# Kernel optimization log

Hardware: AMD Instinct MI355X
Metric: run time of the kernel (lower is better)

The kernel has to match this reference:

```python
import jax, jax.numpy as jnp
import numpy as np
import math

E = 256      # embed_dim
H = 16       # num_heads
D = E // H   # qkv_dim
MSH = 16     # ms_hidden_dim
B, R, C = 2, 512, 512


def setup_inputs() -> dict:
    key = jax.random.key(0)
    ks = jax.random.split(key, 10)
    x1 = jax.random.normal(ks[0], (B, R, E), jnp.float32)
    x2 = jax.random.normal(ks[1], (B, C, E), jnp.float32)
    attn_mask = jax.random.randint(ks[2], (B, R, C), 0, 2) > 0  # True = valid
    cost_mat = jax.random.uniform(ks[3], (B, R, C), jnp.float32)
    # torch nn.Linear default init ~ U(-1/sqrt(fan_in), 1/sqrt(fan_in))
    def lin(k, out_d, in_d, bound):
        return jax.random.uniform(k, (out_d, in_d), jnp.float32, -bound, bound)
    Wqv1 = lin(ks[4], 2 * E, E, 1.0 / math.sqrt(E))
    Wkv2 = lin(ks[5], 2 * E, E, 1.0 / math.sqrt(E))
    W1 = lin(ks[6], H * MSH, 2 * H, math.sqrt(0.5))       # mix1_init
    W2 = lin(ks[7], H, H * MSH, math.sqrt(1.0 / MSH))      # mix2_init
    Wout1 = lin(ks[8], E, E, 1.0 / math.sqrt(E))
    Wout2 = lin(ks[9], E, E, 1.0 / math.sqrt(E))
    return {"x1": x1, "x2": x2, "attn_mask": attn_mask, "cost_mat": cost_mat,
            "Wqv1": Wqv1, "Wkv2": Wkv2, "W1": W1, "W2": W2,
            "Wout1": Wout1, "Wout2": Wout2}


def _apply_weights_and_combine(logits, v, mask):
    # mask: True = masked out; rows fully masked are un-masked (torch clone trick)
    all_masked = jnp.all(mask, axis=-1, keepdims=True)
    mask = jnp.where(all_masked, False, mask)
    logits = jnp.where(mask, -jnp.inf, logits)
    w = jax.nn.softmax(logits, axis=-1)          # [b,h,r,c]
    out = jnp.einsum('bhrc,bhcd->bhrd', w, v)     # [b,h,r,d]
    b, h, r, d = out.shape
    return out.transpose(0, 2, 1, 3).reshape(b, r, h * d)  # b s (h d)


def reference(x1, x2, attn_mask, cost_mat, Wqv1, Wkv2, W1, W2, Wout1, Wout2):
    b, r, _ = x1.shape
    c = x2.shape[1]
    # q, v1 from x1 ; k, v2 from x2
    qv = (x1 @ Wqv1.T).reshape(b, r, 2, H, D)
    q = qv[:, :, 0].transpose(0, 2, 1, 3)   # [b,h,r,d]
    v1 = qv[:, :, 1].transpose(0, 2, 1, 3)
    kv = (x2 @ Wkv2.T).reshape(b, c, 2, H, D)
    k = kv[:, :, 0].transpose(0, 2, 1, 3)   # [b,h,c,d]
    v2 = kv[:, :, 1].transpose(0, 2, 1, 3)

    dot = jnp.einsum('bhrd,bhcd->bhrc', q, k) * (1.0 / math.sqrt(D))
    cost = jnp.broadcast_to(cost_mat[:, None], dot.shape)  # [b,h,r,c]

    # MixedScoreFF: stack -> [b,h,r,c,2] -> [b,r,c,2h] -> MLP -> [b,r,c,h]
    two = jnp.stack((dot, cost), axis=-1)
    two = two.transpose(0, 2, 3, 1, 4).reshape(b, r, c, 2 * H)
    ms = jax.nn.relu(two @ W1.T) @ W2.T      # [b,r,c,H]
    ms1 = ms.transpose(0, 3, 1, 2)            # [b,h,r,c]
    ms2 = ms1.transpose(0, 1, 3, 2)           # [b,h,c,r]

    mask1 = jnp.broadcast_to(~attn_mask[:, None], (b, H, r, c))  # True = masked
    mask2 = mask1.transpose(0, 1, 3, 2)

    h1 = _apply_weights_and_combine(ms1, v2, mask1) @ Wout1.T  # [b,r,E]
    h2 = _apply_weights_and_combine(ms2, v1, mask2) @ Wout2.T  # [b,c,E]
    return (h1, h2)
```

## Files before the change

kernel.cpp:

```cpp
#include <hip/hip_runtime.h>
#include <hip/hip_bf16.h>

typedef unsigned int   u32;
typedef unsigned short u16;

typedef __attribute__((ext_vector_type(8))) short    sh8;
typedef __attribute__((ext_vector_type(4))) float    f32x4;
typedef __attribute__((ext_vector_type(8))) _Float16 f16x8;
typedef __attribute__((ext_vector_type(2))) _Float16 f16x2;
typedef __attribute__((ext_vector_type(2))) __fp16   fp16x2raw;

union F16x8 { f16x8 v; uint4 u; f16x2 p[4]; _Float16 h[8]; };
union F16x4u { uint2 u; _Float16 h[4]; };
union F16x2u { u32 u; _Float16 h[2]; };
union CvtU  { fp16x2raw r; f16x2 p; u32 u; };

__device__ __forceinline__ float b2f(u16 u) { union { u32 i; float f; } v; v.i = ((u32)u) << 16; return v.f; }
__device__ __forceinline__ u16   f2b(float f){
  union { float f; u32 i; } v; v.f = f;
  u32 u = v.i;
  u32 r = (u + 0x7fffu + ((u >> 16) & 1u)) >> 16;
  return (u16)r;
}
__device__ __forceinline__ u32 pk2(float a, float b) {
  __hip_bfloat162 h2 = __float22bfloat162_rn(make_float2(a, b));
  union { __hip_bfloat162 h; u32 u; } v; v.h = h2; return v.u;
}
__device__ __forceinline__ f16x2 cvtpk(float a, float b) {
  CvtU c; c.r = __builtin_amdgcn_cvt_pkrtz(a, b); return c.p;
}
__device__ __forceinline__ u32 cvtpku(float a, float b) {
  CvtU c; c.r = __builtin_amdgcn_cvt_pkrtz(a, b); return c.u;
}

__device__ __forceinline__ f32x4 mfma16(uint4 a, uint4 b, f32x4 c) {
  union { uint4 u; sh8 s; } ua, ub;
  ua.u = a; ub.u = b;
  return __builtin_amdgcn_mfma_f32_16x16x32_bf16(ua.s, ub.s, c, 0, 0, 0);
}
__device__ __forceinline__ f32x4 mfma32h(f16x8 a, f16x8 b, f32x4 c) {
  return __builtin_amdgcn_mfma_f32_16x16x32_f16(a, b, c, 0, 0, 0);
}

__device__ __forceinline__ void split8(float4 v0, float4 v1, uint4& hi, uint4& lo) {
  float a[8] = {v0.x, v0.y, v0.z, v0.w, v1.x, v1.y, v1.z, v1.w};
  u32 hw[4], lw[4];
#pragma unroll
  for (int t = 0; t < 4; t++) {
    u32 hp = pk2(a[2 * t], a[2 * t + 1]);
    float r0 = a[2 * t]     - __uint_as_float(hp << 16);
    float r1 = a[2 * t + 1] - __uint_as_float(hp & 0xffff0000u);
    hw[t] = hp;
    lw[t] = pk2(r0, r1);
  }
  hi = make_uint4(hw[0], hw[1], hw[2], hw[3]);
  lo = make_uint4(lw[0], lw[1], lw[2], lw[3]);
}

__global__ void __launch_bounds__(256)
gemm_mf(const float* __restrict__ A0, const float* __restrict__ B0, float* __restrict__ C0,
        const float* __restrict__ A1, const float* __restrict__ B1, float* __restrict__ C1,
        int N, int K) {
  int t = threadIdx.x, L = t & 63, w = t >> 6;
  int cl = L & 15, q = L >> 4;
  int by = blockIdx.y, sel = by >> 4;
  const float* A  = sel ? A1 : A0;
  const float* Bw = sel ? B1 : B0;
  float*       C  = sel ? C1 : C0;
  int m0 = (by & 15) * 64 + w * 16;
  int n0 = blockIdx.x * 16;

  f32x4 acc; acc[0] = 0.f; acc[1] = 0.f; acc[2] = 0.f; acc[3] = 0.f;
  const float* ar = A  + (size_t)(m0 + cl) * K + 8 * q;
  const float* br = Bw + (size_t)(n0 + cl) * K + 8 * q;

  for (int k0 = 0; k0 < K; k0 += 32) {
    float4 av0 = *(const float4*)(ar + k0);
    float4 av1 = *(const float4*)(ar + k0 + 4);
    float4 bv0 = *(const float4*)(br + k0);
    float4 bv1 = *(const float4*)(br + k0 + 4);
    uint4 ahi, alo, bhi, blo;
    split8(av0, av1, ahi, alo);
    split8(bv0, bv1, bhi, blo);
    acc = mfma16(ahi, bhi, acc);
    acc = mfma16(ahi, blo, acc);
    acc = mfma16(alo, bhi, acc);
  }
#pragma unroll
  for (int i = 0; i < 4; i++)
    C[(size_t)(m0 + 4 * q + i) * N + n0 + cl] = acc[i];
}

__global__ void __launch_bounds__(256)
gemm_mf_pack(const float* __restrict__ x1, const float* __restrict__ Wqv1, u16* __restrict__ vhT1,
             const float* __restrict__ x2, const float* __restrict__ Wkv2, u16* __restrict__ vhT2,
             const float* __restrict__ W1, const float* __restrict__ W2,
             uint4* __restrict__ QQ4, uint4* __restrict__ KH4, uint4* __restrict__ KL4z,
             uint4* __restrict__ W1F8hi, uint4* __restrict__ W1F8lo,
             uint4* __restrict__ W2F8hi, uint4* __restrict__ W2F8lo) {
  __shared__ float Ld[4][16][17];
  int t = threadIdx.x, L = t & 63, w = t >> 6;
  int cl = L & 15, q = L >> 4;
  int by = blockIdx.y;

  if (by == 32) {
    if (blockIdx.x >= 8) return;
    int tid = blockIdx.x * 256 + t;
    if (tid < 1024) {
      int LL = tid & 63, nt = tid >> 6;
      int j = nt * 16 + (LL & 15), qq = LL >> 4;
      F16x8 hi, lo;
#pragma unroll
      for (int jj = 0; jj < 8; jj++) {
        float wv = W1[j * 32 + qq * 8 + jj];
        hi.h[jj] = (_Float16)wv;
        lo.h[jj] = (_Float16)(wv - (float)hi.h[jj]);
      }
      W1F8hi[tid] = hi.u;
      W1F8lo[tid] = lo.u;
    } else if (tid < 1536) {
      int t2 = tid - 1024;
      int LL = t2 & 63, p = t2 >> 6;
      int h = LL & 15, qq = LL >> 4;
      F16x8 hi, lo;
#pragma unroll
      for (int jj = 0; jj < 8; jj++) {
        int j = 32 * p + ((jj >> 2) << 4) + 4 * qq + (jj & 3);
        float wv = W2[h * 256 + j];
        hi.h[jj] = (_Float16)wv;
        lo.h[jj] = (_Float16)(wv - (float)hi.h[jj]);
      }
      W2F8hi[t2] = hi.u;
      W2F8lo[t2] = lo.u;
    }
    return;
  }

  int sel = by >> 4;
  const float* A  = sel ? x2 : x1;
  const float* Bw = sel ? Wkv2 : Wqv1;
  int m0 = (by & 15) * 64 + w * 16;
  int n0 = blockIdx.x * 16;

  f32x4 acc; acc[0] = 0.f; acc[1] = 0.f; acc[2] = 0.f; acc[3] = 0.f;
  const float* ar = A  + (size_t)(m0 + cl) * 256 + 8 * q;
  const float* br = Bw + (size_t)(n0 + cl) * 256 + 8 * q;

  for (int k0 = 0; k0 < 256; k0 += 32) {
    float4 av0 = *(const float4*)(ar + k0);
    float4 av1 = *(const float4*)(ar + k0 + 4);
    float4 bv0 = *(const float4*)(br + k0);
    float4 bv1 = *(const float4*)(br + k0 + 4);
    uint4 ahi, alo, bhi, blo;
    split8(av0, av1, ahi, alo);
    split8(bv0, bv1, bhi, blo);
    acc = mfma16(ahi, bhi, acc);
    acc = mfma16(ahi, blo, acc);
    acc = mfma16(alo, bhi, acc);
  }

  int b = m0 >> 9;
  int row = (m0 & 511) + cl;

  if (n0 >= 256) {
#pragma unroll
    for (int i = 0; i < 4; i++) Ld[w][cl][4 * q + i] = acc[i];
    if (q < 2) {
      float vt[8];
#pragma unroll
      for (int jj = 0; jj < 8; jj++) vt[jj] = Ld[w][cl][q * 8 + jj];
      uint4 o = make_uint4(cvtpku(vt[0], vt[1]), cvtpku(vt[2], vt[3]),
                           cvtpku(vt[4], vt[5]), cvtpku(vt[6], vt[7]));
      u16* vT = sel ? vhT2 : vhT1;
      *(uint4*)(vT + ((size_t)(b * 256) + (n0 - 256) + cl) * 512 + (m0 & 511) + 8 * q) = o;
    }
    return;
  }

#pragma unroll
  for (int i = 0; i < 4; i++) Ld[w][cl][4 * q + i] = acc[i];
  float v[8];
#pragma unroll
  for (int jj = 0; jj < 8; jj++) v[jj] = Ld[w][(q & 1) * 8 + jj][cl];

  int r = row;
  int h = n0 >> 4;

  if (sel == 0) {
    u32 wv[4];
#pragma unroll
    for (int t2 = 0; t2 < 4; t2++) {
      float a  = v[2 * t2] * 0.25f, bb = v[2 * t2 + 1] * 0.25f;
      u32 hp = pk2(a, bb);
      if (q >= 2) {
        float r0 = a  - __uint_as_float(hp << 16);
        float r1 = bb - __uint_as_float(hp & 0xffff0000u);
        wv[t2] = pk2(r0, r1);
      } else wv[t2] = hp;
    }
    QQ4[((size_t)((b * 16 + h) * 4 + q) << 9) + r] = make_uint4(wv[0], wv[1], wv[2], wv[3]);
  } else {
    u32 hw[4], lw[4];
#pragma unroll
    for (int t2 = 0; t2 < 4; t2++) {
      float a = v[2 * t2], bb = v[2 * t2 + 1];
      u32 hp = pk2(a, bb);
      float r0 = a  - __uint_as_float(hp << 16);
      float r1 = bb - __uint_as_float(hp & 0xffff0000u);
      hw[t2] = hp;
      lw[t2] = pk2(r0, r1);
    }
    if (q < 2) {
      KH4[((size_t)((b * 16 + h) * 2 + q) << 9) + r]       = make_uint4(hw[0], hw[1], hw[2], hw[3]);
      KL4z[((size_t)((b * 16 + h) * 4 + 2 + q) << 9) + r]  = make_uint4(0, 0, 0, 0);
    } else {
      KL4z[((size_t)((b * 16 + h) * 4 + (q - 2)) << 9) + r] = make_uint4(lw[0], lw[1], lw[2], lw[3]);
    }
  }
}

__global__ void __launch_bounds__(256, 4)
ms_mfma8c(const uint4* __restrict__ QQ4, const uint4* __restrict__ KH4,
          const uint4* __restrict__ KL4z, const float* __restrict__ cost,
          const uint4* __restrict__ W1F8hi, const uint4* __restrict__ W1F8lo,
          const uint4* __restrict__ W2F8hi, const uint4* __restrict__ W2F8lo,
          u16* __restrict__ ms1, u16* __restrict__ ms2) {
  __shared__ __align__(16) u32 Dl[2 * 2176];
  int t = threadIdx.x, L = t & 63, w = t >> 6;
  int cl = L & 15, q = L >> 4;
  int b = blockIdx.z, c0 = blockIdx.y * 16;
  int pairId = w >> 1, wl = w & 1;
  int r0a = blockIdx.x * 32 + pairId * 16;
  int r0  = r0a + wl * 8;
  u32* D = Dl + pairId * 2176;

  f32x4 z; z[0] = 0.f; z[1] = 0.f; z[2] = 0.f; z[3] = 0.f;

#pragma unroll 2
  for (int hpi = 0; hpi < 4; hpi++) {
    int hp = wl * 4 + hpi;
    int h0 = 2 * hp, h1 = 2 * hp + 1;
    uint4 qa  = QQ4[((size_t)((b * 16 + h0) * 4 + q) << 9) + r0a + cl];
    uint4 qa2 = QQ4[((size_t)((b * 16 + h0) * 4 + (q & 1)) << 9) + r0a + cl];
    uint4 kb1 = KH4[((size_t)((b * 16 + h0) * 2 + (q & 1)) << 9) + c0 + cl];
    uint4 kb2 = KL4z[((size_t)((b * 16 + h0) * 4 + q) << 9) + c0 + cl];
    f32x4 d0 = mfma16(qa, kb1, z);
    d0 = mfma16(qa2, kb2, d0);
    uint4 qb  = QQ4[((size_t)((b * 16 + h1) * 4 + q) << 9) + r0a + cl];
    uint4 qb2 = QQ4[((size_t)((b * 16 + h1) * 4 + (q & 1)) << 9) + r0a + cl];
    uint4 kc1 = KH4[((size_t)((b * 16 + h1) * 2 + (q & 1)) << 9) + c0 + cl];
    uint4 kc2 = KL4z[((size_t)((b * 16 + h1) * 4 + q) << 9) + c0 + cl];
    f32x4 d1 = mfma16(qb, kc1, z);
    d1 = mfma16(qb2, kc2, d1);
#pragma unroll
    for (int i = 0; i < 4; i++)
      D[(4 * q + i) * 136 + hp * 17 + cl] = cvtpku(d0[i], d1[i]);
  }
  __syncthreads();

  F16x8 xv[8];
#pragma unroll
  for (int rr = 0; rr < 8; rr++) {
    int rl = wl * 8 + rr;
    float cv = cost[((size_t)(b * 512) + r0 + rr) * 512 + c0 + cl];
    u32 ch = cvtpku(0.f, cv);
    u32 ua = D[rl * 136 + (2 * q) * 17 + cl];
    u32 ub = D[rl * 136 + (2 * q + 1) * 17 + cl];
    xv[rr].u = make_uint4((ua & 0xffffu) | ch, (ua >> 16) | ch,
                          (ub & 0xffffu) | ch, (ub >> 16) | ch);
  }

  f32x4 acc2[8];
#pragma unroll
  for (int rr = 0; rr < 8; rr++) acc2[rr] = z;

#pragma unroll 1
  for (int p = 0; p < 8; p++) {
    F16x8 w1h0, w1h1, w2h, w2l;
    w1h0.u = W1F8hi[(2 * p) * 64 + L];
    w1h1.u = W1F8hi[(2 * p + 1) * 64 + L];
    w2h.u  = W2F8hi[p * 64 + L];
    w2l.u  = W2F8lo[p * 64 + L];
#pragma unroll
    for (int rr = 0; rr < 8; rr++) {
      f32x4 a0 = mfma32h(w1h0.v, xv[rr].v, z);
      f32x4 a1 = mfma32h(w1h1.v, xv[rr].v, z);
      F16x8 hf;
      hf.p[0] = cvtpk(fmaxf(a0[0], 0.f), fmaxf(a0[1], 0.f));
      hf.p[1] = cvtpk(fmaxf(a0[2], 0.f), fmaxf(a0[3], 0.f));
      hf.p[2] = cvtpk(fmaxf(a1[0], 0.f), fmaxf(a1[1], 0.f));
      hf.p[3] = cvtpk(fmaxf(a1[2], 0.f), fmaxf(a1[3], 0.f));
      acc2[rr] = mfma32h(hf.v, w2h.v, acc2[rr]);
      acc2[rr] = mfma32h(hf.v, w2l.v, acc2[rr]);
    }
  }

  u32* ms1u = (u32*)ms1;
#pragma unroll
  for (int rr = 0; rr < 8; rr++) {
    size_t base = ((size_t)(b * 16 + cl) * 512 + (r0 + rr)) * 256 + (c0 >> 1) + q * 2;
    ms1u[base]     = pk2(acc2[rr][0], acc2[rr][1]);
    ms1u[base + 1] = pk2(acc2[rr][2], acc2[rr][3]);
  }
  u32* ms2u = (u32*)ms2;
#pragma unroll
  for (int i = 0; i < 4; i++) {
    int c = c0 + 4 * q + i;
    u32 o[4];
#pragma unroll
    for (int j = 0; j < 4; j++)
      o[j] = pk2(acc2[2 * j][i], acc2[2 * j + 1][i]);
    size_t base2 = ((size_t)(b * 16 + cl) * 512 + c) * 256 + (r0 >> 1);
    *(uint4*)&ms2u[base2] = make_uint4(o[0], o[1], o[2], o[3]);
  }
}

__global__ void __launch_bounds__(256, 4)
softmax_pv_mf(const u16* __restrict__ ms1s, const u16* __restrict__ ms2s,
              const int* __restrict__ mask,
              const u16* __restrict__ vhT1, const u16* __restrict__ vhT2,
              float* __restrict__ o1, float* __restrict__ o2) {
  __shared__ __align__(16) char pbufc[4][8192];
  __shared__ unsigned char maskbytes[8][64];
  __shared__ float sden[4][8];
  int t = threadIdx.x, L = t & 63, w = t >> 6;
  int cl = L & 15, q = L >> 4;
  int bx = blockIdx.x;
  int u  = (bx & 7) + 8 * ((bx >> 3) & 1);
  int v  = (bx >> 4) & 3;
  int hq = bx >> 6;
  int rt = u * 4 + v;
  int b = blockIdx.y, dir = blockIdx.z;
  int fix0 = rt * 8, h = hq * 4 + w;
  const u16* ms = dir ? ms2s : ms1s;

  if (dir == 0) {
#pragma unroll
    for (int fo = 0; fo < 2; fo++) {
      int f = 2 * w + fo;
      const int* mr = mask + ((size_t)(b * 512) + fix0 + f) * 512 + 8 * L;
      uint4 m0 = *(const uint4*)mr;
      uint4 m1 = *(const uint4*)(mr + 4);
      u32 bits = (u32)(m0.x != 0)        | ((u32)(m0.y != 0) << 1)
               | ((u32)(m0.z != 0) << 2) | ((u32)(m0.w != 0) << 3)
               | ((u32)(m1.x != 0) << 4) | ((u32)(m1.y != 0) << 5)
               | ((u32)(m1.z != 0) << 6) | ((u32)(m1.w != 0) << 7);
      maskbytes[f][L] = (unsigned char)bits;
    }
  } else {
    u32 b0 = 0, b1 = 0;
#pragma unroll
    for (int j = 0; j < 8; j++) {
      const int* mp = mask + ((size_t)(b * 512) + 8 * L + j) * 512 + fix0 + 2 * w;
      uint2 mv = *(const uint2*)mp;
      b0 |= (u32)(mv.x != 0) << j;
      b1 |= (u32)(mv.y != 0) << j;
    }
    maskbytes[2 * w][L]     = (unsigned char)b0;
    maskbytes[2 * w + 1][L] = (unsigned char)b1;
  }
  __syncthreads();

  const u16* msbase = ms + ((size_t)((b * 16 + h) * 512) + fix0) * 512 + 8 * L;
  uint4 pre[8];
#pragma unroll
  for (int f = 0; f < 8; f++) pre[f] = *(const uint4*)(msbase + f * 512);

  char* pb = pbufc[w];
#pragma unroll
  for (int f = 0; f < 8; f++) {
    u32 uw[4] = {pre[f].x, pre[f].y, pre[f].z, pre[f].w};
    float lg[8];
#pragma unroll
    for (int j = 0; j < 4; j++) {
      lg[2 * j]     = __uint_as_float(uw[j] << 16);
      lg[2 * j + 1] = __uint_as_float(uw[j] & 0xffff0000u);
    }
    u32 mb = (u32)maskbytes[f][L];
    bool um = (__ballot(mb != 0) != 0ULL);
    u32 eff = um ? mb : 0xffu;
    float mx = -3.4e38f;
#pragma unroll
    for (int j = 0; j < 8; j++)
      mx = fmaxf(mx, ((eff >> j) & 1) ? lg[j] : -3.4e38f);
    for (int off = 32; off; off >>= 1) mx = fmaxf(mx, __shfl_xor(mx, off));
    float s = 0.f; u32 pw[4];
#pragma unroll
    for (int j = 0; j < 4; j++) {
      float p0 = ((eff >> (2 * j)) & 1)     ? __expf(lg[2 * j]     - mx) : 0.f;
      float p1 = ((eff >> (2 * j + 1)) & 1) ? __expf(lg[2 * j + 1] - mx) : 0.f;
      s += p0 + p1;
      pw[j] = cvtpku(p0, p1);
    }
    for (int off = 32; off; off >>= 1) s += __shfl_xor(s, off);
    if (L == 0) sden[w][f] = s;
    *(uint4*)(pb + f * 1024 + ((16 * L) ^ (f << 4))) = make_uint4(pw[0], pw[1], pw[2], pw[3]);
  }

  const u16* vT = (dir ? vhT1 : vhT2) + ((size_t)(b * 256 + h * 16 + cl) * 512) + 8 * q;
  f32x4 accA; accA[0] = 0.f; accA[1] = 0.f; accA[2] = 0.f; accA[3] = 0.f;
  f32x4 accB = accA;
  int ar = (cl & 7);
#pragma unroll
  for (int kk = 0; kk < 16; kk++) {
    F16x8 pa, vb;
    pa.u = *(const uint4*)(pb + ar * 1024 + (((kk << 6) + (q << 4)) ^ (ar << 4)));
    vb.u = *(const uint4*)(vT + (kk << 5));
    if (kk & 1) accB = mfma32h(pa.v, vb.v, accB);
    else        accA = mfma32h(pa.v, vb.v, accA);
  }

  if (q < 2) {
    float* obuf = dir ? o2 : o1;
#pragma unroll
    for (int i = 0; i < 4; i++) {
      int f = 4 * q + i;
      float inv = 1.f / sden[w][f];
      obuf[((size_t)(b * 512) + fix0 + f) * 256 + h * 16 + cl] = (accA[i] + accB[i]) * inv;
    }
  }
}

extern "C" void kernel_launch(void* const* d_in, const int* in_sizes, int n_in,
                              void* d_out, int out_size, void* d_ws, size_t ws_size,
                              hipStream_t stream) {
  const float* x1    = (const float*)d_in[0];
  const float* x2    = (const float*)d_in[1];
  const int*   attn  = (const int*)d_in[2];
  const float* cost  = (const float*)d_in[3];
  const float* Wqv1  = (const float*)d_in[4];
  const float* Wkv2  = (const float*)d_in[5];
  const float* W1    = (const float*)d_in[6];
  const float* W2    = (const float*)d_in[7];
  const float* Wout1 = (const float*)d_in[8];
  const float* Wout2 = (const float*)d_in[9];
  float* out = (float*)d_out;

  char* ws = (char*)d_ws;
  uint4* W1F8hi = (uint4*)(ws);
  uint4* W1F8lo = (uint4*)(ws + (16 << 10));
  uint4* W2F8hi = (uint4*)(ws + (32 << 10));
  uint4* W2F8lo = (uint4*)(ws + (40 << 10));
  u16*   vhT1 = (u16*)(ws + (64 << 10));
  u16*   vhT2 = (u16*)(ws + (64 << 10) + (512 << 10));
  u16*   ms1 = (u16*)(ws + (64 << 10) + (4 << 20));
  u16*   ms2 = (u16*)(ws + (64 << 10) + (20 << 20));
  char*  tail= (ws + (64 << 10) + (36 << 20));
  uint4* QQ4  = (uint4*)(tail);
  uint4* KH4  = (uint4*)(tail + (1 << 20));
  uint4* KL4z = (uint4*)(tail + (1 << 20) + (512 << 10));
  float* o1  = (float*)(tail + (3 << 20));
  float* o2  = (float*)(tail + (4 << 20));

  gemm_mf_pack<<<dim3(32, 33), 256, 0, stream>>>(x1, Wqv1, vhT1, x2, Wkv2, vhT2,
                                                 W1, W2, QQ4, KH4, KL4z,
                                                 W1F8hi, W1F8lo, W2F8hi, W2F8lo);

  ms_mfma8c<<<dim3(16, 32, 2), 256, 0, stream>>>(QQ4, KH4, KL4z, cost,
                                                 W1F8hi, W1F8lo, W2F8hi, W2F8lo, ms1, ms2);

  softmax_pv_mf<<<dim3(256, 2, 2), 256, 0, stream>>>(ms1, ms2, attn, vhT1, vhT2, o1, o2);

  gemm_mf<<<dim3(16, 32), 256, 0, stream>>>(o1, Wout1, out, o2, Wout2, out + (size_t)262144, 256, 256);
}
```

Before: 141.9 us.

## Fuse softmax-PV with output projection into single kernel

Merges the softmax/PV kernel and the output projection GEMM into one kernel. Each 512-thread block now handles all 16 heads for 8 rows, looping over two heads per wave. It stores the normalized attention output as bf16 hi/lo pairs in shared memory and then does the Wout projection from there. This removes one launch and the fp32 o1/o2 round trip through global memory. In exchange the grid drops from 1024 to 256 blocks, and each block re-reads the full Wout matrix, which may hurt occupancy and parallelism.

```diff
diff --git a/kernel.cpp b/kernel.cpp
--- a/kernel.cpp
+++ b/kernel.cpp
@@ -55,40 +55,6 @@
   }
   hi = make_uint4(hw[0], hw[1], hw[2], hw[3]);
   lo = make_uint4(lw[0], lw[1], lw[2], lw[3]);
-}
-
-__global__ void __launch_bounds__(256)
-gemm_mf(const float* __restrict__ A0, const float* __restrict__ B0, float* __restrict__ C0,
-        const float* __restrict__ A1, const float* __restrict__ B1, float* __restrict__ C1,
-        int N, int K) {
-  int t = threadIdx.x, L = t & 63, w = t >> 6;
-  int cl = L & 15, q = L >> 4;
-  int by = blockIdx.y, sel = by >> 4;
-  const float* A  = sel ? A1 : A0;
-  const float* Bw = sel ? B1 : B0;
-  float*       C  = sel ? C1 : C0;
-  int m0 = (by & 15) * 64 + w * 16;
-  int n0 = blockIdx.x * 16;
-
-  f32x4 acc; acc[0] = 0.f; acc[1] = 0.f; acc[2] = 0.f; acc[3] = 0.f;
-  const float* ar = A  + (size_t)(m0 + cl) * K + 8 * q;
-  const float* br = Bw + (size_t)(n0 + cl) * K + 8 * q;
-
-  for (int k0 = 0; k0 < K; k0 += 32) {
-    float4 av0 = *(const float4*)(ar + k0);
-    float4 av1 = *(const float4*)(ar + k0 + 4);
-    float4 bv0 = *(const float4*)(br + k0);
-    float4 bv1 = *(const float4*)(br + k0 + 4);
-    uint4 ahi, alo, bhi, blo;
-    split8(av0, av1, ahi, alo);
-    split8(bv0, bv1, bhi, blo);
-    acc = mfma16(ahi, bhi, acc);
-    acc = mfma16(ahi, blo, acc);
-    acc = mfma16(alo, bhi, acc);
-  }
-#pragma unroll
-  for (int i = 0; i < 4; i++)
-    C[(size_t)(m0 + 4 * q + i) * N + n0 + cl] = acc[i];
 }
 
 __global__ void __launch_bounds__(256)
@@ -315,108 +281,136 @@
   }
 }
 
-__global__ void __launch_bounds__(256, 4)
-softmax_pv_mf(const u16* __restrict__ ms1s, const u16* __restrict__ ms2s,
-              const int* __restrict__ mask,
-              const u16* __restrict__ vhT1, const u16* __restrict__ vhT2,
-              float* __restrict__ o1, float* __restrict__ o2) {
-  __shared__ __align__(16) char pbufc[4][8192];
+__global__ void __launch_bounds__(512, 4)
+softmax_pv_out(const u16* __restrict__ ms1s, const u16* __restrict__ ms2s,
+               const int* __restrict__ mask,
+               const u16* __restrict__ vhT1, const u16* __restrict__ vhT2,
+               const float* __restrict__ Wout1, const float* __restrict__ Wout2,
+               float* __restrict__ out) {
+  __shared__ __align__(16) char pbufc[8][8192];
   __shared__ unsigned char maskbytes[8][64];
-  __shared__ float sden[4][8];
+  __shared__ float sden[8][8];
+  __shared__ __align__(16) u16 ohi[8][264];
+  __shared__ __align__(16) u16 olo[8][264];
   int t = threadIdx.x, L = t & 63, w = t >> 6;
   int cl = L & 15, q = L >> 4;
   int bx = blockIdx.x;
   int u  = (bx & 7) + 8 * ((bx >> 3) & 1);
-  int v  = (bx >> 4) & 3;
-  int hq = bx >> 6;
-  int rt = u * 4 + v;
+  int v  = bx >> 4;
   int b = blockIdx.y, dir = blockIdx.z;
-  int fix0 = rt * 8, h = hq * 4 + w;
+  int fix0 = (u * 4 + v) * 8;
   const u16* ms = dir ? ms2s : ms1s;
 
   if (dir == 0) {
-#pragma unroll
-    for (int fo = 0; fo < 2; fo++) {
-      int f = 2 * w + fo;
-      const int* mr = mask + ((size_t)(b * 512) + fix0 + f) * 512 + 8 * L;
-      uint4 m0 = *(const uint4*)mr;
-      uint4 m1 = *(const uint4*)(mr + 4);
-      u32 bits = (u32)(m0.x != 0)        | ((u32)(m0.y != 0) << 1)
-               | ((u32)(m0.z != 0) << 2) | ((u32)(m0.w != 0) << 3)
-               | ((u32)(m1.x != 0) << 4) | ((u32)(m1.y != 0) << 5)
-               | ((u32)(m1.z != 0) << 6) | ((u32)(m1.w != 0) << 7);
-      maskbytes[f][L] = (unsigned char)bits;
-    }
+    const int* mr = mask + ((size_t)(b * 512) + fix0 + w) * 512 + 8 * L;
+    uint4 m0 = *(const uint4*)mr;
+    uint4 m1 = *(const uint4*)(mr + 4);
+    u32 bits = (u32)(m0.x != 0)        | ((u32)(m0.y != 0) << 1)
+             | ((u32)(m0.z != 0) << 2) | ((u32)(m0.w != 0) << 3)
+             | ((u32)(m1.x != 0) << 4) | ((u32)(m1.y != 0) << 5)
+             | ((u32)(m1.z != 0) << 6) | ((u32)(m1.w != 0) << 7);
+    maskbytes[w][L] = (unsigned char)bits;
   } else {
-    u32 b0 = 0, b1 = 0;
+    u32 b0 = 0;
 #pragma unroll
     for (int j = 0; j < 8; j++) {
-      const int* mp = mask + ((size_t)(b * 512) + 8 * L + j) * 512 + fix0 + 2 * w;
-      uint2 mv = *(const uint2*)mp;
-      b0 |= (u32)(mv.x != 0) << j;
-      b1 |= (u32)(mv.y != 0) << j;
-    }
-    maskbytes[2 * w][L]     = (unsigned char)b0;
-    maskbytes[2 * w + 1][L] = (unsigned char)b1;
+      int mv = mask[((size_t)(b * 512) + 8 * L + j) * 512 + fix0 + w];
+      b0 |= (u32)(mv != 0) << j;
+    }
+    maskbytes[w][L] = (unsigned char)b0;
   }
   __syncthreads();
 
-  const u16* msbase = ms + ((size_t)((b * 16 + h) * 512) + fix0) * 512 + 8 * L;
-  uint4 pre[8];
-#pragma unroll
-  for (int f = 0; f < 8; f++) pre[f] = *(const uint4*)(msbase + f * 512);
-
+  f32x4 z; z[0] = 0.f; z[1] = 0.f; z[2] = 0.f; z[3] = 0.f;
   char* pb = pbufc[w];
-#pragma unroll
-  for (int f = 0; f < 8; f++) {
-    u32 uw[4] = {pre[f].x, pre[f].y, pre[f].z, pre[f].w};
-    float lg[8];
-#pragma unroll
-    for (int j = 0; j < 4; j++) {
-      lg[2 * j]     = __uint_as_float(uw[j] << 16);
-      lg[2 * j + 1] = __uint_as_float(uw[j] & 0xffff0000u);
-    }
-    u32 mb = (u32)maskbytes[f][L];
-    bool um = (__ballot(mb != 0) != 0ULL);
-    u32 eff = um ? mb : 0xffu;
-    float mx = -3.4e38f;
-#pragma unroll
-    for (int j = 0; j < 8; j++)
-      mx = fmaxf(mx, ((eff >> j) & 1) ? lg[j] : -3.4e38f);
-    for (int off = 32; off; off >>= 1) mx = fmaxf(mx, __shfl_xor(mx, off));
-    float s = 0.f; u32 pw[4];
-#pragma unroll
-    for (int j = 0; j < 4; j++) {
-      float p0 = ((eff >> (2 * j)) & 1)     ? __expf(lg[2 * j]     - mx) : 0.f;
-      float p1 = ((eff >> (2 * j + 1)) & 1) ? __expf(lg[2 * j + 1] - mx) : 0.f;
-      s += p0 + p1;
-      pw[j] = cvtpku(p0, p1);
-    }
-    for (int off = 32; off; off >>= 1) s += __shfl_xor(s, off);
-    if (L == 0) sden[w][f] = s;
-    *(uint4*)(pb + f * 1024 + ((16 * L) ^ (f << 4))) = make_uint4(pw[0], pw[1], pw[2], pw[3]);
-  }
-
-  const u16* vT = (dir ? vhT1 : vhT2) + ((size_t)(b * 256 + h * 16 + cl) * 512) + 8 * q;
-  f32x4 accA; accA[0] = 0.f; accA[1] = 0.f; accA[2] = 0.f; accA[3] = 0.f;
-  f32x4 accB = accA;
-  int ar = (cl & 7);
-#pragma unroll
-  for (int kk = 0; kk < 16; kk++) {
-    F16x8 pa, vb;
-    pa.u = *(const uint4*)(pb + ar * 1024 + (((kk << 6) + (q << 4)) ^ (ar << 4)));
-    vb.u = *(const uint4*)(vT + (kk << 5));
-    if (kk & 1) accB = mfma32h(pa.v, vb.v, accB);
-    else        accA = mfma32h(pa.v, vb.v, accA);
-  }
-
-  if (q < 2) {
-    float* obuf = dir ? o2 : o1;
-#pragma unroll
-    for (int i = 0; i < 4; i++) {
-      int f = 4 * q + i;
-      float inv = 1.f / sden[w][f];
-      obuf[((size_t)(b * 512) + fix0 + f) * 256 + h * 16 + cl] = (accA[i] + accB[i]) * inv;
+
+#pragma unroll 1
+  for (int hh = 0; hh < 2; hh++) {
+    int h = w + 8 * hh;
+
+    const u16* msbase = ms + ((size_t)((b * 16 + h) * 512) + fix0) * 512 + 8 * L;
+    uint4 pre[8];
+#pragma unroll
+    for (int f = 0; f < 8; f++) pre[f] = *(const uint4*)(msbase + f * 512);
+
+#pragma unroll
+    for (int f = 0; f < 8; f++) {
+      u32 uw[4] = {pre[f].x, pre[f].y, pre[f].z, pre[f].w};
+      float lg[8];
+#pragma unroll
+      for (int j = 0; j < 4; j++) {
+        lg[2 * j]     = __uint_as_float(uw[j] << 16);
+        lg[2 * j + 1] = __uint_as_float(uw[j] & 0xffff0000u);
+      }
+      u32 mb = (u32)maskbytes[f][L];
+      bool um = (__ballot(mb != 0) != 0ULL);
+      u32 eff = um ? mb : 0xffu;
+      float mx = -3.4e38f;
+#pragma unroll
+      for (int j = 0; j < 8; j++)
+        mx = fmaxf(mx, ((eff >> j) & 1) ? lg[j] : -3.4e38f);
+      for (int off = 32; off; off >>= 1) mx = fmaxf(mx, __shfl_xor(mx, off));
+      float s = 0.f; u32 pw[4];
+#pragma unroll
+      for (int j = 0; j < 4; j++) {
+        float p0 = ((eff >> (2 * j)) & 1)     ? __expf(lg[2 * j]     - mx) : 0.f;
+        float p1 = ((eff >> (2 * j + 1)) & 1) ? __expf(lg[2 * j + 1] - mx) : 0.f;
+        s += p0 + p1;
+        pw[j] = cvtpku(p0, p1);
+      }
+      for (int off = 32; off; off >>= 1) s += __shfl_xor(s, off);
+      if (L == 0) sden[w][f] = s;
+      *(uint4*)(pb + f * 1024 + ((16 * L) ^ (f << 4))) = make_uint4(pw[0], pw[1], pw[2], pw[3]);
+    }
+
+    const u16* vT = (dir ? vhT1 : vhT2) + ((size_t)(b * 256 + h * 16 + cl) * 512) + 8 * q;
+    f32x4 accA = z, accB = z;
+    int ar = (cl & 7);
+#pragma unroll
+    for (int kk = 0; kk < 16; kk++) {
+      F16x8 pa, vb;
+      pa.u = *(const uint4*)(pb + ar * 1024 + (((kk << 6) + (q << 4)) ^ (ar << 4)));
+      vb.u = *(const uint4*)(vT + (kk << 5));
+      if (kk & 1) accB = mfma32h(pa.v, vb.v, accB);
+      else        accA = mfma32h(pa.v, vb.v, accA);
+    }
+
+    if (q < 2) {
+#pragma unroll
+      for (int i = 0; i < 4; i++) {
+        int f = 4 * q + i;
+        float inv = 1.f / sden[w][f];
+        float val = (accA[i] + accB[i]) * inv;
+        u16 hv = f2b(val);
+        ohi[f][h * 16 + cl] = hv;
+        olo[f][h * 16 + cl] = f2b(val - b2f(hv));
+      }
+    }
+  }
+  __syncthreads();
+
+  const float* Wo = dir ? Wout2 : Wout1;
+  float* ob = out + (size_t)dir * 262144 + ((size_t)(b * 512) + fix0) * 256;
+#pragma unroll 1
+  for (int nt = w; nt < 16; nt += 8) {
+    int n0 = nt * 16;
+    const float* br = Wo + (size_t)(n0 + cl) * 256 + 8 * q;
+    f32x4 acc = z;
+    for (int k0 = 0; k0 < 256; k0 += 32) {
+      uint4 Ahi = *(const uint4*)&ohi[cl & 7][8 * q + k0];
+      uint4 Alo = *(const uint4*)&olo[cl & 7][8 * q + k0];
+      float4 bv0 = *(const float4*)(br + k0);
+      float4 bv1 = *(const float4*)(br + k0 + 4);
+      uint4 bhi, blo;
+      split8(bv0, bv1, bhi, blo);
+      acc = mfma16(Ahi, bhi, acc);
+      acc = mfma16(Ahi, blo, acc);
+      acc = mfma16(Alo, bhi, acc);
+    }
+    if (q < 2) {
+#pragma unroll
+      for (int i = 0; i < 4; i++)
+        ob[(size_t)(4 * q + i) * 256 + n0 + cl] = acc[i];
     }
   }
 }
@@ -449,8 +443,6 @@
   uint4* QQ4  = (uint4*)(tail);
   uint4* KH4  = (uint4*)(tail + (1 << 20));
   uint4* KL4z = (uint4*)(tail + (1 << 20) + (512 << 10));
-  float* o1  = (float*)(tail + (3 << 20));
-  float* o2  = (float*)(tail + (4 << 20));
 
   gemm_mf_pack<<<dim3(32, 33), 256, 0, stream>>>(x1, Wqv1, vhT1, x2, Wkv2, vhT2,
                                                  W1, W2, QQ4, KH4, KL4z,
@@ -459,7 +451,6 @@
   ms_mfma8c<<<dim3(16, 32, 2), 256, 0, stream>>>(QQ4, KH4, KL4z, cost,
                                                  W1F8hi, W1F8lo, W2F8hi, W2F8lo, ms1, ms2);
 
-  softmax_pv_mf<<<dim3(256, 2, 2), 256, 0, stream>>>(ms1, ms2, attn, vhT1, vhT2, o1, o2);
-
-  gemm_mf<<<dim3(16, 32), 256, 0, stream>>>(o1, Wout1, out, o2, Wout2, out + (size_t)262144, 256, 256);
-}
+  softmax_pv_out<<<dim3(64, 2, 2), 512, 0, stream>>>(ms1, ms2, attn, vhT1, vhT2,
+                                                     Wout1, Wout2, out);
+}
```

New measurement: 146.1 us. 3.0% more time.
